# Kernel tuning notes

Measured on AMD Instinct MI355X. Metric: run time of the kernel, lower is better.

The kernel has to match this reference:

```python
import jax, jax.numpy as jnp
import numpy as np

N_HEADS = 71
HEAD_DIM = 64
ROPE_BASE = 10000.0
SCALE = 1.0 / np.sqrt(HEAD_DIM)  # 0.125


def setup_inputs() -> dict:
    key = jax.random.key(0)
    k1, k2, k3 = jax.random.split(key, 3)
    B, S, H = 1, 1024, N_HEADS * HEAD_DIM  # 4544
    F = (N_HEADS + 2) * HEAD_DIM           # 4672 fused QKV out features
    hidden_states = jax.random.normal(k1, (B, 1, S, H), dtype=jnp.float32)
    qkv_weight = jax.random.normal(k2, (H, F), dtype=jnp.float32) * 0.02
    dense_weight = jax.random.normal(k3, (H, H), dtype=jnp.float32) * 0.02
    # additive causal mask [1,1,S,S]
    causal = np.tril(np.ones((S, S), dtype=bool))
    attention_mask = jnp.asarray(np.where(causal, 0.0, -1e9).astype(np.float32))[None, None]
    return {"hidden_states": hidden_states, "qkv_weight": qkv_weight,
            "dense_weight": dense_weight, "attention_mask": attention_mask}


def _rope_tables(seq_len):
    inv_freq = 1.0 / (ROPE_BASE ** (jnp.arange(0, HEAD_DIM, 2, dtype=jnp.float32) / HEAD_DIM))
    t = jnp.arange(seq_len, dtype=jnp.float32)
    freqs = t[:, None] * inv_freq[None, :]          # [S, 32]
    emb = jnp.concatenate([freqs, freqs], axis=-1)  # [S, 64]
    return jnp.cos(emb), jnp.sin(emb)


def _rotate_half(x):
    h = HEAD_DIM // 2
    return jnp.concatenate([-x[..., h:], x[..., :h]], axis=-1)


def reference(hidden_states, qkv_weight, dense_weight, attention_mask):
    # Prefill: hidden_states [B, 1, S, H]
    B, _, S, H = hidden_states.shape
    x = hidden_states[:, 0]                                  # [B, S, H]
    qkv = jnp.einsum('bsh,hf->bsf', x, qkv_weight)           # fused QKV matmul
    qd = N_HEADS * HEAD_DIM
    # Falcon-7B MQA head split: 71 query heads, 1 shared K and V head
    q = qkv[..., :qd].reshape(B, S, N_HEADS, HEAD_DIM).transpose(0, 2, 1, 3)  # [B, nH, S, d]
    k = qkv[..., qd:qd + HEAD_DIM]                           # [B, S, d]
    v = qkv[..., qd + HEAD_DIM:]                             # [B, S, d]
    cos, sin = _rope_tables(S)                               # [S, d]
    q = q * cos + _rotate_half(q) * sin
    k = k * cos + _rotate_half(k) * sin
    scores = jnp.einsum('bhqd,bkd->bhqk', q, k) * SCALE      # [B, nH, S, S]
    scores = scores + attention_mask                         # causal mask (alibi is None for Falcon-7B)
    probs = jax.nn.softmax(scores, axis=-1)
    ctx = jnp.einsum('bhqk,bkd->bhqd', probs, v)             # [B, nH, S, d]
    merged = ctx.transpose(0, 2, 1, 3).reshape(B, S, H)      # concat heads
    out = jnp.einsum('bsh,hf->bsf', merged, dense_weight)    # selfout dense
    return out[:, None]                                      # [B, 1, S, H]
```

## Files before the change

### kernel.cpp

```cpp
#include <hip/hip_runtime.h>
#include <hip/hip_bf16.h>

#define DI __device__ __forceinline__

typedef __attribute__((ext_vector_type(8))) short bf16x8;
typedef __attribute__((ext_vector_type(4))) float f32x4;
typedef __attribute__((ext_vector_type(4))) short s16x4;

constexpr int S  = 1024;
constexpr int NH = 71;
constexpr int HD = 64;
constexpr int H  = NH * HD;
constexpr int F  = (NH + 2) * HD;
constexpr float K2 = 0.125f * 1.44269504f;

DI short f2bf(float f) {
  union { float f; unsigned u; } v; v.f = f;
  unsigned r = v.u + 0x7fffu + ((v.u >> 16) & 1u);
  return (short)(r >> 16);
}
DI unsigned cvt_pk_bf16(float lo, float hi) {
  unsigned r;
  asm("v_cvt_pk_bf16_f32 %0, %1, %2" : "=v"(r) : "v"(lo), "v"(hi));
  return r;
}
DI float redmax_g(float x) {
  float y = fmaxf(x, __int_as_float(__builtin_amdgcn_ds_swizzle(__float_as_int(x), 0x401F)));
  return fmaxf(y, __shfl_xor(y, 32));
}
DI float redsum_g(float x) {
  float y = x + __int_as_float(__builtin_amdgcn_ds_swizzle(__float_as_int(x), 0x401F));
  return y + __shfl_xor(y, 32);
}

DI void gload_lds16(const void* g, void* l) {
  __builtin_amdgcn_global_load_lds(
      (const __attribute__((address_space(1))) unsigned int*)g,
      (__attribute__((address_space(3))) unsigned int*)l, 16, 0, 0);
}

DI bf16x8 ldswz(const char* base, int row, int slot) {
  return *(const bf16x8*)(base + row * 128 + ((slot ^ (row & 7)) << 4));
}

__global__ void cast_x_kernel(const float* __restrict__ x, short* __restrict__ xb, int n4) {
  int i = blockIdx.x * blockDim.x + threadIdx.x;
  if (i >= n4) return;
  f32x4 v = ((const f32x4*)x)[i];
  s16x4 o = { f2bf(v.x), f2bf(v.y), f2bf(v.z), f2bf(v.w) };
  ((s16x4*)xb)[i] = o;
}

__global__ __launch_bounds__(256) void transpose2_kernel(
    const float* __restrict__ W1, short* __restrict__ Wt1,
    const float* __restrict__ W2, short* __restrict__ Wt2) {
  __shared__ float tf[64 * 64];
  __shared__ short tb[64 * 72];
  const int nb1 = (F / 64) * (H / 64);
  int bid = blockIdx.x;
  const float* W; short* Wt; int N, n0, k0;
  if (bid < nb1) {
    W = W1; Wt = Wt1; N = F;
    n0 = (bid % (F / 64)) * 64; k0 = (bid / (F / 64)) * 64;
  } else {
    bid -= nb1;
    W = W2; Wt = Wt2; N = H;
    n0 = (bid % (H / 64)) * 64; k0 = (bid / (H / 64)) * 64;
  }
  const int t = threadIdx.x;
  const int lane = t & 63, wave = t >> 6;
  char* tfb = (char*)tf;
  char* tbb = (char*)tb;

#pragma unroll
  for (int i = 0; i < 4; ++i) {
    int row = (i * 4 + wave) * 4 + (lane >> 4);
    gload_lds16(W + (size_t)(k0 + row) * N + n0 + (lane & 15) * 4,
                tfb + (i * 4 + wave) * 1024);
  }
  __syncthreads();

#pragma unroll
  for (int pass = 0; pass < 2; ++pass) {
    int m = wave + 4 * pass;
    int n = lane;
    float v[8];
#pragma unroll
    for (int i = 0; i < 8; ++i)
      v[i] = tf[(8 * m + i) * 64 + n];
    uint4 wv;
    wv.x = cvt_pk_bf16(v[0], v[1]);
    wv.y = cvt_pk_bf16(v[2], v[3]);
    wv.z = cvt_pk_bf16(v[4], v[5]);
    wv.w = cvt_pk_bf16(v[6], v[7]);
    int sp = (m + (n >> 2)) & 7;
    *(uint4*)(tbb + n * 144 + sp * 16) = wv;
  }
  __syncthreads();

#pragma unroll
  for (int pass = 0; pass < 2; ++pass) {
    int u = pass * 256 + t;
    int n = u >> 3, m = u & 7;
    int sp = (m + (n >> 2)) & 7;
    bf16x8 vv = *(const bf16x8*)(tbb + n * 144 + sp * 16);
    *(bf16x8*)(Wt + (size_t)(n0 + n) * H + k0 + 8 * m) = vv;
  }
}

__global__ __launch_bounds__(256) void rope_pack_kernel(
    const float* __restrict__ qkv,
    short* __restrict__ Qb, short* __restrict__ Kb, short* __restrict__ Vt) {
  __shared__ float cs[32], sn[32];
  int s = blockIdx.x;
  if (threadIdx.x < 32) {
    float invf = powf(10000.0f, -(float)threadIdx.x / 32.0f);
    float a = (float)s * invf;
    cs[threadIdx.x] = cosf(a);
    sn[threadIdx.x] = sinf(a);
  }
  __syncthreads();
  const float* row = qkv + (size_t)s * F;
  for (int q4 = threadIdx.x; q4 < F / 4; q4 += 256) {
    int c = q4 * 4;
    int hh = c >> 6, d = c & 63;
    f32x4 v = *(const f32x4*)(row + c);
    if (hh <= NH) {
      f32x4 r = *(const f32x4*)(row + c + ((d < 32) ? 32 : -32));
      float sgn = (d < 32) ? -1.0f : 1.0f;
      int i0 = d & 31;
      s16x4 o;
#pragma unroll
      for (int j = 0; j < 4; ++j)
        o[j] = f2bf(v[j] * cs[i0 + j] + sgn * r[j] * sn[i0 + j]);
      if (hh < NH) *(s16x4*)(Qb + ((size_t)hh * S + s) * 64 + d) = o;
      else         *(s16x4*)(Kb + (size_t)s * 64 + d) = o;
    } else {
#pragma unroll
      for (int j = 0; j < 4; ++j)
        Vt[(size_t)(d + j) * S + s] = f2bf(v[j]);
    }
  }
}

__global__ __launch_bounds__(256, 3) void gemm_bt_kernel(
    const short* __restrict__ A, const short* __restrict__ Bt, float* __restrict__ C,
    int M, int N, int K) {
  __shared__ short As[2 * 128 * 64];
  __shared__ short Bs[2 * 64 * 64];
  const int tid = threadIdx.x;
  const int lane = tid & 63;
  const int wave = tid >> 6;
  const int wr = wave >> 1, wc = wave & 1;
  const int lr = lane & 15, g = lane >> 4;

  const int nwg = gridDim.x;
  int bid = blockIdx.x;
  int wgid = ((nwg & 7) == 0) ? ((bid & 7) * (nwg >> 3) + (bid >> 3)) : bid;
  const int ntm = M >> 7;
  const int tn = wgid / ntm;
  const int tm = wgid % ntm;

  f32x4 acc[4][2] = {};

  int srowA[4], skofA[4];
#pragma unroll
  for (int iss = 0; iss < 4; ++iss) {
    int d = iss * 256 + wave * 64 + lane;
    int row = (d >> 2) & 127;
    int c = (d & 3) ^ ((row >> 1) & 3);
    srowA[iss] = row;
    skofA[iss] = ((d >> 9) << 5) + c * 8;
  }
  int srowB[2], skofB[2];
#pragma unroll
  for (int iss = 0; iss < 2; ++iss) {
    int d = iss * 256 + wave * 64 + lane;
    int row = (d >> 2) & 63;
    int c = (d & 3) ^ ((row >> 1) & 3);
    srowB[iss] = row;
    skofB[iss] = ((d >> 8) << 5) + c * 8;
  }
  int offA[2][4], offB[2][2];
#pragma unroll
  for (int im = 0; im < 4; ++im) {
    int row_a = wr * 64 + im * 16 + lr;
    int sl = (g ^ ((row_a >> 1) & 3)) << 4;
#pragma unroll
    for (int kk = 0; kk < 2; ++kk) offA[kk][im] = kk * 8192 + row_a * 64 + sl;
  }
#pragma unroll
  for (int in = 0; in < 2; ++in) {
    int row_b = wc * 32 + in * 16 + lr;
    int sl = (g ^ ((row_b >> 1) & 3)) << 4;
#pragma unroll
    for (int kk = 0; kk < 2; ++kk) offB[kk][in] = kk * 4096 + row_b * 64 + sl;
  }

  char* AsB = (char*)As;
  char* BsB = (char*)Bs;
  const size_t Abase = (size_t)tm * 128 * K;
  const size_t Bbase = (size_t)tn * 64 * K;

#define STAGE(buf, k0)                                                                  \
  {                                                                                     \
    _Pragma("unroll")                                                                   \
    for (int iss = 0; iss < 4; ++iss)                                                   \
      gload_lds16(A + Abase + (size_t)srowA[iss] * K + (k0) + skofA[iss],               \
                  AsB + (buf) * 16384 + (iss * 4 + wave) * 1024);                       \
    _Pragma("unroll")                                                                   \
    for (int iss = 0; iss < 2; ++iss)                                                   \
      gload_lds16(Bt + Bbase + (size_t)srowB[iss] * K + (k0) + skofB[iss],              \
                  BsB + (buf) * 8192 + (iss * 4 + wave) * 1024);                        \
  }

  STAGE(0, 0);
  __syncthreads();
  const int KS = K >> 6;
  for (int t = 0; t < KS; ++t) {
    const int cur = t & 1;
    if (t + 1 < KS) STAGE(cur ^ 1, (t + 1) << 6);
    const char* Ac = AsB + cur * 16384;
    const char* Bc = BsB + cur * 8192;
    bf16x8 af[2][4], bfr[2][2];
#pragma unroll
    for (int kk = 0; kk < 2; ++kk) {
#pragma unroll
      for (int im = 0; im < 4; ++im) af[kk][im] = *(const bf16x8*)(Ac + offA[kk][im]);
#pragma unroll
      for (int in = 0; in < 2; ++in) bfr[kk][in] = *(const bf16x8*)(Bc + offB[kk][in]);
    }
#pragma unroll
    for (int kk = 0; kk < 2; ++kk)
#pragma unroll
      for (int im = 0; im < 4; ++im)
#pragma unroll
        for (int in = 0; in < 2; ++in)
          acc[im][in] = __builtin_amdgcn_mfma_f32_16x16x32_bf16(af[kk][im], bfr[kk][in], acc[im][in], 0, 0, 0);
    __syncthreads();
  }
#undef STAGE

#pragma unroll
  for (int im = 0; im < 4; ++im) {
#pragma unroll
    for (int in = 0; in < 2; ++in) {
      int row = tm * 128 + wr * 64 + im * 16 + g * 4;
      int col = tn * 64 + wc * 32 + in * 16 + lr;
#pragma unroll
      for (int i = 0; i < 4; ++i)
        C[(size_t)(row + i) * N + col] = acc[im][in][i];
    }
  }
}

DI void attn_step(const char* Kc, const char* Vc, char* P,
                  int key0, int qrow, bf16x8 aQ0, bf16x8 aQ1,
                  f32x4* accO, float& m, float& l, int lr, int g) {
  f32x4 p[4];
#pragma unroll
  for (int nf = 0; nf < 4; ++nf) {
    int row = nf * 16 + lr;
    bf16x8 k0 = ldswz(Kc, row, g);
    bf16x8 k1 = ldswz(Kc, row, g + 4);
    f32x4 z = {};
    z = __builtin_amdgcn_mfma_f32_16x16x32_bf16(k0, aQ0, z, 0, 0, 0);
    p[nf] = __builtin_amdgcn_mfma_f32_16x16x32_bf16(k1, aQ1, z, 0, 0, 0);
  }
  float pmx = -3e30f;
#pragma unroll
  for (int nf = 0; nf < 4; ++nf)
#pragma unroll
    for (int i = 0; i < 4; ++i) {
      int key = key0 + nf * 16 + 4 * g + i;
      float sv = p[nf][i] * K2 + (key <= qrow ? 0.0f : -1e30f);
      p[nf][i] = sv;
      pmx = fmaxf(pmx, sv);
    }
  float pm = redmax_g(pmx);
  float mn = fmaxf(m, pm);
  float scl = __builtin_exp2f(m - mn);
  m = mn;
  float rsx = 0.f;
#pragma unroll
  for (int nf = 0; nf < 4; ++nf) {
    f32x4 pe;
#pragma unroll
    for (int i = 0; i < 4; ++i) {
      pe[i] = __builtin_exp2f(p[nf][i] - m);
      rsx += pe[i];
    }
    uint2 wv;
    wv.x = cvt_pk_bf16(pe[0], pe[1]);
    wv.y = cvt_pk_bf16(pe[2], pe[3]);
    *(uint2*)(P + lr * 144 + nf * 32 + g * 8) = wv;
  }
  float rs = redsum_g(rsx);
  l = l * scl + rs;
#pragma unroll
  for (int df = 0; df < 4; ++df)
#pragma unroll
    for (int i = 0; i < 4; ++i)
      accO[df][i] *= scl;
#pragma unroll
  for (int st = 0; st < 2; ++st) {
    bf16x8 bP = *(const bf16x8*)(P + lr * 144 + st * 64 + g * 16);
#pragma unroll
    for (int df = 0; df < 4; ++df) {
      bf16x8 aV = ldswz(Vc, df * 16 + lr, g + 4 * st);
      accO[df] = __builtin_amdgcn_mfma_f32_16x16x32_bf16(aV, bP, accO[df], 0, 0, 0);
    }
  }
}

__global__ __launch_bounds__(256) void attn_kernel(
    const short* __restrict__ Qb,
    const short* __restrict__ Kb,
    const short* __restrict__ Vt,
    short* __restrict__ merged) {
  __shared__ short Ks[2][4096];
  __shared__ short Vs[2][4096];
  __shared__ short Ps[4][16 * 72];
  const int lane = threadIdx.x & 63, w = threadIdx.x >> 6;
  const int lr = lane & 15, g = lane >> 4;
  const int j = blockIdx.x, head = blockIdx.y;
  const int kbmax = 15 - j;
  const int qA = j * 64 + w * 16 + lr;
  const int qB = (15 - j) * 64 + w * 16 + lr;
  char* KsB = (char*)Ks;
  char* VsB = (char*)Vs;
  char* P = (char*)Ps[w];

  int crow[2], cslot[2];
#pragma unroll
  for (int i = 0; i < 2; ++i) {
    int c = (i * 4 + w) * 64 + lane;
    crow[i] = c >> 3;
    cslot[i] = (c & 7) ^ (crow[i] & 7);
  }

  const short* qap = Qb + ((size_t)head * S + qA) * 64 + g * 8;
  bf16x8 aQA0 = *(const bf16x8*)(qap);
  bf16x8 aQA1 = *(const bf16x8*)(qap + 32);
  const short* qbp = Qb + ((size_t)head * S + qB) * 64 + g * 8;
  bf16x8 aQB0 = *(const bf16x8*)(qbp);
  bf16x8 aQB1 = *(const bf16x8*)(qbp + 32);

  f32x4 accA[4] = {}, accB[4] = {};
  float mA = -3e30f, lA = 0.f, mB = -3e30f, lB = 0.f;

#define STAGEKV(buf, key0)                                                       \
  {                                                                              \
    _Pragma("unroll")                                                            \
    for (int i = 0; i < 2; ++i) {                                                \
      gload_lds16(Kb + (size_t)((key0) + crow[i]) * 64 + cslot[i] * 8,           \
                  KsB + (buf) * 8192 + (i * 4 + w) * 1024);                      \
      gload_lds16(Vt + (size_t)crow[i] * S + (key0) + cslot[i] * 8,              \
                  VsB + (buf) * 8192 + (i * 4 + w) * 1024);                      \
    }                                                                            \
  }

  STAGEKV(0, 0);
  for (int kb = 0; kb <= kbmax; ++kb) {
    const int cur = kb & 1;
    __syncthreads();
    if (kb < kbmax) STAGEKV(cur ^ 1, (kb + 1) * 64);
    const char* Kc = KsB + cur * 8192;
    const char* Vc = VsB + cur * 8192;
    attn_step(Kc, Vc, P, kb * 64, qB, aQB0, aQB1, accB, mB, lB, lr, g);
    if (kb <= j)
      attn_step(Kc, Vc, P, kb * 64, qA, aQA0, aQA1, accA, mA, lA, lr, g);
  }
#undef STAGEKV

  float rlA = 1.0f / lA, rlB = 1.0f / lB;
#pragma unroll
  for (int df = 0; df < 4; ++df)
#pragma unroll
    for (int i = 0; i < 4; ++i) {
      int d = head * 64 + df * 16 + 4 * g + i;
      merged[(size_t)qB * H + d] = f2bf(accB[df][i] * rlB);
      merged[(size_t)qA * H + d] = f2bf(accA[df][i] * rlA);
    }
}

extern "C" void kernel_launch(void* const* d_in, const int* in_sizes, int n_in,
                              void* d_out, int out_size, void* d_ws, size_t ws_size,
                              hipStream_t stream) {
  const float* x    = (const float*)d_in[0];
  const float* wqkv = (const float*)d_in[1];
  const float* wd   = (const float*)d_in[2];
  float* out = (float*)d_out;

  char* ws = (char*)d_ws;
  size_t off = 0;
  short* Wqkvt  = (short*)(ws + off); off += (size_t)F * H * 2;
  short* Wdt    = (short*)(ws + off); off += (size_t)H * H * 2;
  short* Qb     = (short*)(ws + off); off += (size_t)NH * S * HD * 2;
  short* Kb     = (short*)(ws + off); off += (size_t)S * HD * 2;
  short* Vtb    = (short*)(ws + off); off += (size_t)HD * S * 2;
  short* merged = (short*)(ws + off); off += (size_t)S * H * 2;
  short* xb     = (short*)(ws + off); off += (size_t)S * H * 2;
  float* qkv    = (float*)(ws + off); off += (size_t)S * F * 4;
  (void)ws_size; (void)in_sizes; (void)n_in; (void)out_size;

  hipLaunchKernelGGL(cast_x_kernel, dim3((S * H / 4 + 255) / 256), dim3(256), 0, stream,
                     x, xb, S * H / 4);
  hipLaunchKernelGGL(transpose2_kernel,
                     dim3((F / 64) * (H / 64) + (H / 64) * (H / 64)), dim3(256), 0, stream,
                     wqkv, Wqkvt, wd, Wdt);
  hipLaunchKernelGGL(gemm_bt_kernel, dim3((F / 64) * (S / 128)), dim3(256), 0, stream,
                     xb, Wqkvt, qkv, S, F, H);
  hipLaunchKernelGGL(rope_pack_kernel, dim3(S), dim3(256), 0, stream,
                     qkv, Qb, Kb, Vtb);
  hipLaunchKernelGGL(attn_kernel, dim3(8, NH), dim3(256), 0, stream,
                     Qb, Kb, Vtb, merged);
  hipLaunchKernelGGL(gemm_bt_kernel, dim3((H / 64) * (S / 128)), dim3(256), 0, stream,
                     merged, Wdt, out, S, H, H);
}
```

Before: 224.7 us.

## Make weight transpose kernel persistent with double-buffered LDS prefetch

The weight transpose/cast kernel now runs as a fixed grid of 2048 blocks that stride over all 64x64 tiles, instead of one block per tile. Each block double-buffers the fp32 input tile in LDS: it issues the asynchronous global-to-LDS load for the next tile, then converts and stores the current one. The intent is to hide global load latency behind the bf16 conversion and writeback, and to save block launch overhead. In exchange each block uses more LDS, which can lower occupancy, and the manual vmcnt waits and barriers make the code more fragile.

```diff
diff --git a/kernel.cpp b/kernel.cpp
--- a/kernel.cpp
+++ b/kernel.cpp
@@ -14,6 +14,11 @@
 constexpr int F  = (NH + 2) * HD;
 constexpr float K2 = 0.125f * 1.44269504f;
 
+constexpr int NT1 = (F / 64) * (H / 64);
+constexpr int NT2 = (H / 64) * (H / 64);
+constexpr int NTT = NT1 + NT2;
+constexpr int TGRID = 2048;
+
 DI short f2bf(float f) {
   union { float f; unsigned u; } v; v.f = f;
   unsigned r = v.u + 0x7fffu + ((v.u >> 16) & 1u);
@@ -51,61 +56,87 @@
   ((s16x4*)xb)[i] = o;
 }
 
+DI void t2_decode(int tile,
+                  const float* W1, short* Wt1, const float* W2, short* Wt2,
+                  const float*& W, short*& Wt, int& N, int& n0, int& k0) {
+  if (tile < NT1) {
+    W = W1; Wt = Wt1; N = F;
+    n0 = (tile % (F / 64)) * 64; k0 = (tile / (F / 64)) * 64;
+  } else {
+    int u = tile - NT1;
+    W = W2; Wt = Wt2; N = H;
+    n0 = (u % (H / 64)) * 64; k0 = (u / (H / 64)) * 64;
+  }
+}
+
 __global__ __launch_bounds__(256) void transpose2_kernel(
     const float* __restrict__ W1, short* __restrict__ Wt1,
     const float* __restrict__ W2, short* __restrict__ Wt2) {
-  __shared__ float tf[64 * 64];
+  __shared__ float tf[2][64 * 64];
   __shared__ short tb[64 * 72];
-  const int nb1 = (F / 64) * (H / 64);
-  int bid = blockIdx.x;
-  const float* W; short* Wt; int N, n0, k0;
-  if (bid < nb1) {
-    W = W1; Wt = Wt1; N = F;
-    n0 = (bid % (F / 64)) * 64; k0 = (bid / (F / 64)) * 64;
-  } else {
-    bid -= nb1;
-    W = W2; Wt = Wt2; N = H;
-    n0 = (bid % (H / 64)) * 64; k0 = (bid / (H / 64)) * 64;
-  }
   const int t = threadIdx.x;
   const int lane = t & 63, wave = t >> 6;
   char* tfb = (char*)tf;
   char* tbb = (char*)tb;
 
-#pragma unroll
-  for (int i = 0; i < 4; ++i) {
-    int row = (i * 4 + wave) * 4 + (lane >> 4);
-    gload_lds16(W + (size_t)(k0 + row) * N + n0 + (lane & 15) * 4,
-                tfb + (i * 4 + wave) * 1024);
-  }
-  __syncthreads();
-
-#pragma unroll
-  for (int pass = 0; pass < 2; ++pass) {
-    int m = wave + 4 * pass;
-    int n = lane;
-    float v[8];
-#pragma unroll
-    for (int i = 0; i < 8; ++i)
-      v[i] = tf[(8 * m + i) * 64 + n];
-    uint4 wv;
-    wv.x = cvt_pk_bf16(v[0], v[1]);
-    wv.y = cvt_pk_bf16(v[2], v[3]);
-    wv.z = cvt_pk_bf16(v[4], v[5]);
-    wv.w = cvt_pk_bf16(v[6], v[7]);
-    int sp = (m + (n >> 2)) & 7;
-    *(uint4*)(tbb + n * 144 + sp * 16) = wv;
-  }
-  __syncthreads();
-
-#pragma unroll
-  for (int pass = 0; pass < 2; ++pass) {
-    int u = pass * 256 + t;
-    int n = u >> 3, m = u & 7;
-    int sp = (m + (n >> 2)) & 7;
-    bf16x8 vv = *(const bf16x8*)(tbb + n * 144 + sp * 16);
-    *(bf16x8*)(Wt + (size_t)(n0 + n) * H + k0 + 8 * m) = vv;
-  }
+#define T2STAGE(buf, tile)                                                        \
+  {                                                                               \
+    const float* W_; short* Wt_; int N_, n0_, k0_;                                \
+    t2_decode((tile), W1, Wt1, W2, Wt2, W_, Wt_, N_, n0_, k0_);                   \
+    _Pragma("unroll")                                                             \
+    for (int i = 0; i < 4; ++i) {                                                 \
+      int row = (i * 4 + wave) * 4 + (lane >> 4);                                 \
+      gload_lds16(W_ + (size_t)(k0_ + row) * N_ + n0_ + (lane & 15) * 4,          \
+                  tfb + (buf) * 16384 + (i * 4 + wave) * 1024);                   \
+    }                                                                             \
+  }
+
+  const int tile0 = blockIdx.x;
+  if (tile0 < NTT) T2STAGE(0, tile0);
+  int buf = 0;
+  for (int tile = tile0; tile < NTT; tile += TGRID) {
+    const int nxt = tile + TGRID;
+    if (nxt < NTT) T2STAGE(buf ^ 1, nxt);
+    if (nxt < NTT) asm volatile("s_waitcnt vmcnt(4)" ::: "memory");
+    else           asm volatile("s_waitcnt vmcnt(0)" ::: "memory");
+    __builtin_amdgcn_sched_barrier(0);
+    __builtin_amdgcn_s_barrier();
+    __builtin_amdgcn_sched_barrier(0);
+
+    const float* tfc = tf[buf];
+#pragma unroll
+    for (int pass = 0; pass < 2; ++pass) {
+      int m = wave + 4 * pass;
+      int n = lane;
+      float v[8];
+#pragma unroll
+      for (int i = 0; i < 8; ++i)
+        v[i] = tfc[(8 * m + i) * 64 + n];
+      uint4 wv;
+      wv.x = cvt_pk_bf16(v[0], v[1]);
+      wv.y = cvt_pk_bf16(v[2], v[3]);
+      wv.z = cvt_pk_bf16(v[4], v[5]);
+      wv.w = cvt_pk_bf16(v[6], v[7]);
+      int sp = (m + (n >> 2)) & 7;
+      *(uint4*)(tbb + n * 144 + sp * 16) = wv;
+    }
+    __syncthreads();
+
+    {
+      const float* W_; short* Wt_; int N_, n0_, k0_;
+      t2_decode(tile, W1, Wt1, W2, Wt2, W_, Wt_, N_, n0_, k0_);
+#pragma unroll
+      for (int pass = 0; pass < 2; ++pass) {
+        int u = pass * 256 + t;
+        int n = u >> 3, m = u & 7;
+        int sp = (m + (n >> 2)) & 7;
+        bf16x8 vv = *(const bf16x8*)(tbb + n * 144 + sp * 16);
+        *(bf16x8*)(Wt_ + (size_t)(n0_ + n) * H + k0_ + 8 * m) = vv;
+      }
+    }
+    buf ^= 1;
+  }
+#undef T2STAGE
 }
 
 __global__ __launch_bounds__(256) void rope_pack_kernel(
@@ -406,8 +437,7 @@
 
   hipLaunchKernelGGL(cast_x_kernel, dim3((S * H / 4 + 255) / 256), dim3(256), 0, stream,
                      x, xb, S * H / 4);
-  hipLaunchKernelGGL(transpose2_kernel,
-                     dim3((F / 64) * (H / 64) + (H / 64) * (H / 64)), dim3(256), 0, stream,
+  hipLaunchKernelGGL(transpose2_kernel, dim3(TGRID), dim3(256), 0, stream,
                      wqkv, Wqkvt, wd, Wdt);
   hipLaunchKernelGGL(gemm_bt_kernel, dim3((F / 64) * (S / 128)), dim3(256), 0, stream,
                      xb, Wqkvt, qkv, S, F, H);
```

New measurement: 227.8 us. About the same (+1.4%).
